# Performance work log

Hardware: AMD Instinct MI355X
Metric: run time of the kernel (lower is better)

## Reference

```python
import jax, jax.numpy as jnp
from jax import lax
import numpy as np

T, B, E, DENSE = 2048, 32, 512, 512
THRESH = 1.0
TAIL_MIN_W = 0.6
EPS = 1e-10


def setup_inputs() -> dict:
    key = jax.random.key(0)
    k1, k2, k3, k4 = jax.random.split(key, 4)
    encoder_raw_out = jax.random.normal(k1, (T, B, E), dtype=jnp.float32)  # T x B x C
    lengths = jax.random.randint(k2, (B,), T // 2, T + 1)
    padding_mask = jnp.arange(T)[None, :] >= lengths[:, None]  # [B,T], True = padding
    # xavier-uniform inits matching torch Linear helper
    s1 = float(np.sqrt(6.0 / (E + DENSE)))
    s2 = float(np.sqrt(6.0 / (DENSE + 1)))
    dense_w = jax.random.uniform(k3, (E, DENSE), jnp.float32, -s1, s1)
    dense_b = jnp.zeros((DENSE,), jnp.float32)
    wproj_w = jax.random.uniform(k4, (DENSE, 1), jnp.float32, -s2, s2)
    wproj_b = jnp.zeros((1,), jnp.float32)
    return dict(encoder_raw_out=encoder_raw_out, padding_mask=padding_mask,
                dense_w=dense_w, dense_b=dense_b, wproj_w=wproj_w, wproj_b=wproj_b)


def _cif(encoder_raw_out, padding_mask, dense_w, dense_b, wproj_w, wproj_b):
    x = jnp.transpose(encoder_raw_out, (1, 0, 2))  # [B,T,E]
    not_pad = ~padding_mask                         # [B,T]
    # produce_weight_type == 'dense'
    h = jax.nn.relu(jnp.einsum('bte,eu->btu', x, dense_w) + dense_b)
    weight = jax.nn.sigmoid(jnp.einsum('btu,uo->bto', h, wproj_w) + wproj_b)[..., 0]
    weight = weight * not_pad.astype(weight.dtype)  # [B,T]
    padding_start = not_pad.sum(-1)                 # [B] int

    def step(carry, inp):
        prev_w, prev_s = carry          # [B], [B,E]
        w_i, x_i, i = inp               # [B], [B,E], scalar
        fired = (prev_w + w_i) >= THRESH            # [B]
        remained = 1.0 - prev_w
        cur_w = jnp.where(fired, w_i - remained, w_i + prev_w)
        f = fired[:, None]
        cur_s = jnp.where(f, (w_i - remained)[:, None] * x_i,
                          prev_s + w_i[:, None] * x_i)
        fired_s = jnp.where(f, prev_s + remained[:, None] * x_i, 0.0)
        # tail handling (eval mode): at first padded frame, emit leftover if weighty enough
        at_tail = (i == padding_start)[:, None]
        tail_s = jnp.where(cur_w[:, None] <= TAIL_MIN_W, 0.0,
                           cur_s / (cur_w[:, None] + EPS))
        fired_s = jnp.where(at_tail, tail_s, fired_s)
        fired_s = jnp.where((i > padding_start)[:, None], 0.0, fired_s)
        return (cur_w, cur_s), fired_s

    init = (jnp.zeros((x.shape[0],), x.dtype), jnp.zeros_like(x[:, 0, :]))
    xs = (jnp.transpose(weight), encoder_raw_out, jnp.arange(x.shape[1]))
    _, fired_states = lax.scan(step, init, xs)          # [T,B,E]
    fired_states = jnp.transpose(fired_states, (1, 0, 2))  # [B,T,E]

    fired_marks = (jnp.abs(fired_states).sum(-1) != 0.0).astype(jnp.int32)  # [B,T]
    # left-pack fired states (non-fired rows are exact zeros, so they pad the tail)
    order = jnp.argsort(1 - fired_marks, axis=1, stable=True)               # [B,T]
    cif_out = jnp.take_along_axis(fired_states, order[:, :, None], axis=1)  # [B,T,E]
    cif_out_padding_mask = (jnp.abs(cif_out).sum(-1) != 0.0).astype(jnp.int32)
    quantity_out = weight.sum(-1)  # eval: org_weight == weight
    return cif_out, cif_out_padding_mask, quantity_out, fired_marks


def reference(encoder_raw_out, padding_mask, dense_w, dense_b, wproj_w, wproj_b):
    return _cif(encoder_raw_out, padding_mask, dense_w, dense_b, wproj_w, wproj_b)
```

## Files before the change

kernel.cpp:

```cpp
#include <hip/hip_runtime.h>
#include <math.h>

#define TT 2048
#define BB 32
#define EE 512
#define NN 512

typedef short bf16x8 __attribute__((ext_vector_type(8)));
typedef float f32x4 __attribute__((ext_vector_type(4)));

__device__ __forceinline__ short bf16_rne(float x) {
    const unsigned u = __float_as_uint(x);
    return (short)((u + 0x7FFFu + ((u >> 16) & 1u)) >> 16);
}
__device__ __forceinline__ float bf16_f32(short h) {
    return __uint_as_float(((unsigned)(unsigned short)h) << 16);
}
__device__ __forceinline__ void gload_lds16(const void* g, void* l) {
    __builtin_amdgcn_global_load_lds((const __attribute__((address_space(1))) void*)g,
                                     (__attribute__((address_space(3))) void*)l, 16, 0, 0);
}

__global__ void detect_mask_kernel(const unsigned* __restrict__ pm, int* __restrict__ flag) {
    __shared__ int s[1024];
    const int l = threadIdx.x;
    int bad = 0;
    for (int i = l; i < BB * TT; i += 1024) bad |= (pm[i] > 1u);
    s[l] = bad;
    __syncthreads();
    for (int st = 512; st > 0; st >>= 1) { if (l < st) s[l] |= s[l + st]; __syncthreads(); }
    if (l == 0) *flag = s[0];
}

__device__ __forceinline__ int pad_at(const void* pm, int idx, int isByte) {
    return isByte ? (int)(((const unsigned char*)pm)[idx] != 0)
                  : (int)(((const int*)pm)[idx] != 0);
}

__global__ void compute_ps_kernel(const void* __restrict__ pm, const int* __restrict__ flag,
                                  int* __restrict__ ps) {
    __shared__ int s[256];
    const int b = blockIdx.x, l = threadIdx.x;
    const int isByte = *flag;
    int cnt = 0;
    for (int t = l; t < TT; t += 256) cnt += (pad_at(pm, b * TT + t, isByte) == 0);
    s[l] = cnt;
    __syncthreads();
    for (int st = 128; st > 0; st >>= 1) { if (l < st) s[l] += s[l + st]; __syncthreads(); }
    if (l == 0) ps[b] = s[0];
}

__global__ __launch_bounds__(256) void split_w_kernel(const float* __restrict__ W,
                                                      short* __restrict__ Wh,
                                                      short* __restrict__ Wl) {
    __shared__ float tile[32][33];
    const int bn = blockIdx.x, bk = blockIdx.y;
    const int tx = threadIdx.x & 31, ty = threadIdx.x >> 5;
    for (int i = ty; i < 32; i += 8)
        tile[i][tx] = W[(size_t)(bk * 32 + i) * NN + bn * 32 + tx];
    __syncthreads();
    for (int i = ty; i < 32; i += 8) {
        const float val = tile[tx][i];
        const short h = bf16_rne(val);
        const short lo = bf16_rne(val - bf16_f32(h));
        const size_t o = (size_t)(bn * 32 + i) * EE + bk * 32 + tx;
        Wh[o] = h;
        Wl[o] = lo;
    }
}

__global__ __launch_bounds__(256, 2) void gemm_weight_mfma(
    const float* __restrict__ x, const void* __restrict__ pm, const int* __restrict__ flag,
    const short* __restrict__ Wh, const short* __restrict__ Wl,
    const float* __restrict__ bias, const float* __restrict__ v, const float* __restrict__ vb,
    float* __restrict__ weight_bt) {
    __shared__ __align__(16) short Ah[128 * 64];
    __shared__ __align__(16) short Al[128 * 64];
    __shared__ __align__(16) short Bh[128 * 64];
    __shared__ __align__(16) short Bl[128 * 64];
    __shared__ float bias_s[512], v_s[512];
    __shared__ float lsum[128][2];

    const int tid = threadIdx.x;
    const int l = tid & 63, wid = tid >> 6;
    const int wr = wid >> 1, wc = wid & 1;
    const int q = l >> 4, li = l & 15, x7 = l & 7;
    const int tp = blockIdx.x;

    for (int i = tid; i < 512; i += 256) { bias_s[i] = bias[i]; v_s[i] = v[i]; }

    const float* xblk = x + (size_t)tp * 128 * EE;
    const int arow = tid >> 1;
    const int akoff = (tid & 1) * 32;
    const int ac0 = akoff >> 3;
    const int aswz = arow & 7;

    float rowsum[4][4];
#pragma unroll
    for (int m = 0; m < 4; ++m)
#pragma unroll
        for (int r = 0; r < 4; ++r) rowsum[m][r] = 0.f;

    for (int nc = 0; nc < 4; ++nc) {
        const int n0 = nc * 128;
        f32x4 acc[4][4];
#pragma unroll
        for (int m = 0; m < 4; ++m)
#pragma unroll
            for (int n = 0; n < 4; ++n) acc[m][n] = (f32x4){0.f, 0.f, 0.f, 0.f};

        for (int k0 = 0; k0 < EE; k0 += 64) {
            __syncthreads();
#pragma unroll
            for (int i = 0; i < 4; ++i) {
                const int u = i * 256 + tid;
                const int row = u >> 3, c = u & 7;
                const int ge = (n0 + row) * EE + k0 + ((c ^ (row & 7)) << 3);
                gload_lds16(Wh + ge, &Bh[u * 8]);
                gload_lds16(Wl + ge, &Bl[u * 8]);
            }
            const float* xr = xblk + (size_t)arow * EE + k0 + akoff;
#pragma unroll
            for (int g = 0; g < 4; ++g) {
                float e[8];
                *(float4*)&e[0] = *(const float4*)&xr[g * 8];
                *(float4*)&e[4] = *(const float4*)&xr[g * 8 + 4];
                bf16x8 hv, lv;
#pragma unroll
                for (int j = 0; j < 8; ++j) {
                    const short h = bf16_rne(e[j]);
                    hv[j] = h;
                    lv[j] = bf16_rne(e[j] - bf16_f32(h));
                }
                const int p = arow * 64 + (((ac0 + g) ^ aswz) << 3);
                *(bf16x8*)&Ah[p] = hv;
                *(bf16x8*)&Al[p] = lv;
            }
            __syncthreads();
#pragma unroll
            for (int kf = 0; kf < 2; ++kf) {
                const int co = (((kf << 2) + q) ^ x7) << 3;
                bf16x8 ah[4], al[4];
#pragma unroll
                for (int m = 0; m < 4; ++m) {
                    const int ro = (wr * 64 + m * 16 + li) * 64 + co;
                    ah[m] = *(const bf16x8*)&Ah[ro];
                    al[m] = *(const bf16x8*)&Al[ro];
                }
#pragma unroll
                for (int n = 0; n < 4; ++n) {
                    const int bo = (wc * 64 + n * 16 + li) * 64 + co;
                    const bf16x8 bh = *(const bf16x8*)&Bh[bo];
                    const bf16x8 bl = *(const bf16x8*)&Bl[bo];
#pragma unroll
                    for (int m = 0; m < 4; ++m) {
                        acc[m][n] = __builtin_amdgcn_mfma_f32_16x16x32_bf16(ah[m], bh, acc[m][n], 0, 0, 0);
                        acc[m][n] = __builtin_amdgcn_mfma_f32_16x16x32_bf16(al[m], bh, acc[m][n], 0, 0, 0);
                        acc[m][n] = __builtin_amdgcn_mfma_f32_16x16x32_bf16(ah[m], bl, acc[m][n], 0, 0, 0);
                    }
                }
            }
        }
#pragma unroll
        for (int m = 0; m < 4; ++m)
#pragma unroll
            for (int n = 0; n < 4; ++n) {
                const int col = n0 + wc * 64 + n * 16 + li;
                const float bcol = bias_s[col], vcol = v_s[col];
#pragma unroll
                for (int r = 0; r < 4; ++r) {
                    const float h = fmaxf(acc[m][n][r] + bcol, 0.f);
                    rowsum[m][r] = fmaf(h, vcol, rowsum[m][r]);
                }
            }
    }
#pragma unroll
    for (int m = 0; m < 4; ++m)
#pragma unroll
        for (int r = 0; r < 4; ++r) {
            float s = rowsum[m][r];
            s += __shfl_xor(s, 1, 64);
            s += __shfl_xor(s, 2, 64);
            s += __shfl_xor(s, 4, 64);
            s += __shfl_xor(s, 8, 64);
            rowsum[m][r] = s;
        }
    if (li == 0) {
#pragma unroll
        for (int m = 0; m < 4; ++m)
#pragma unroll
            for (int r = 0; r < 4; ++r)
                lsum[wr * 64 + m * 16 + q * 4 + r][wc] = rowsum[m][r];
    }
    __syncthreads();
    if (tid < 128) {
        const int isByte = *flag;
        const float logit = lsum[tid][0] + lsum[tid][1] + *vb;
        const float wg = 1.0f / (1.0f + expf(-logit));
        const int gr = tp * 128 + tid;
        const int t = gr >> 5, b = gr & 31;
        weight_bt[(size_t)b * TT + t] = pad_at(pm, b * TT + t, isByte) ? 0.f : wg;
    }
}

#define BAND 5e-5f
#define MAXEV 32
__global__ __launch_bounds__(64) void cif_scan_kernel(
    float* __restrict__ weight_bt,
    const float* __restrict__ x, const float* __restrict__ W,
    const float* __restrict__ bias, const float* __restrict__ v,
    const float* __restrict__ vb,
    float* __restrict__ cseq_g) {
    __shared__ __align__(16) float wsm[TT];
    __shared__ __align__(16) float cseq[TT];
    __shared__ __align__(16) float xrow[EE];
    __shared__ int evl_s[MAXEV];
    __shared__ float wfix_s[MAXEV];
    __shared__ unsigned fixedbm[TT / 32];
    const int b = blockIdx.x, l = threadIdx.x;
    float* wrow = weight_bt + (size_t)b * TT;

    for (int t = l * 8; t < TT; t += 64 * 8) {
        *(float4*)&wsm[t]     = *(const float4*)&wrow[t];
        *(float4*)&wsm[t + 4] = *(const float4*)&wrow[t + 4];
    }
    fixedbm[l] = 0u;
    __syncthreads();

    int t0s = 0;
    for (int iter = 0; iter < 64; ++iter) {
        if (l == 0) {
            float c = (t0s > 0) ? cseq[t0s - 1] : 0.f;
            float4 n1a = *(const float4*)&wsm[t0s];
            float4 n1b = *(const float4*)&wsm[t0s + 4];
            const int tp8 = (t0s + 8) & (TT - 1);
            float4 n2a = *(const float4*)&wsm[tp8];
            float4 n2b = *(const float4*)&wsm[tp8 + 4];
            for (int t = t0s; t < TT; t += 8) {
                const float4 wa = n1a, wb = n1b;
                n1a = n2a; n1b = n2b;
                const int tn = (t + 16) & (TT - 1);
                n2a = *(const float4*)&wsm[tn];
                n2b = *(const float4*)&wsm[tn + 4];
                const float wv[8] = {wa.x, wa.y, wa.z, wa.w, wb.x, wb.y, wb.z, wb.w};
                float cs[8];
#pragma unroll
                for (int u = 0; u < 8; ++u) {
                    const float w = wv[u];
                    const float a = 1.0f - c;
                    const float s = c + w;
                    const float bb = w - a;
                    c = (s >= 1.0f) ? bb : s;
                    cs[u] = c;
                }
                *(float4*)&cseq[t]     = make_float4(cs[0], cs[1], cs[2], cs[3]);
                *(float4*)&cseq[t + 4] = make_float4(cs[4], cs[5], cs[6], cs[7]);
            }
        }
        __syncthreads();
        const int base = l * 32;
        const unsigned fixw = fixedbm[l];
        unsigned hm = 0u;
        for (int u = 0; u < 32; ++u) {
            const int t = base + u;
            const float w = wsm[t];
            if (w > 0.f && !((fixw >> u) & 1u)) {
                const float cprev = t ? cseq[t - 1] : 0.f;
                if (fabsf(cprev + w - 1.0f) < BAND) hm |= (1u << u);
            }
        }
        unsigned long long bal = __ballot(hm != 0u);
        int nev = 0;
        while (bal != 0ull && nev < MAXEV) {
            const int src = __ffsll((unsigned long long)bal) - 1;
            unsigned hs = __shfl(hm, src, 64);
            while (hs != 0u && nev < MAXEV) {
                const int u = __ffs(hs) - 1;
                if (l == 0) evl_s[nev] = src * 32 + u;
                ++nev;
                hs &= hs - 1u;
            }
            bal &= bal - 1ull;
        }
        __syncthreads();
        if (nev == 0) break;
        const float4 v0 = *(const float4*)&v[l * 8];
        const float4 v1 = *(const float4*)&v[l * 8 + 4];
        const float4 bi0 = *(const float4*)&bias[l * 8];
        const float4 bi1 = *(const float4*)&bias[l * 8 + 4];
        for (int k = 0; k < nev; ++k) {
            const int ev = evl_s[k];
            const float* xr = &x[((size_t)ev * BB + b) * EE];
            *(float4*)&xrow[l * 8]     = *(const float4*)&xr[l * 8];
            *(float4*)&xrow[l * 8 + 4] = *(const float4*)&xr[l * 8 + 4];
            __syncthreads();
            float h[8] = {bi0.x, bi0.y, bi0.z, bi0.w, bi1.x, bi1.y, bi1.z, bi1.w};
#pragma unroll 4
            for (int e = 0; e < EE; ++e) {
                const float xe = xrow[e];
                const float4 w0 = *(const float4*)&W[(size_t)e * NN + l * 8];
                const float4 w1 = *(const float4*)&W[(size_t)e * NN + l * 8 + 4];
                h[0] = fmaf(xe, w0.x, h[0]); h[1] = fmaf(xe, w0.y, h[1]);
                h[2] = fmaf(xe, w0.z, h[2]); h[3] = fmaf(xe, w0.w, h[3]);
                h[4] = fmaf(xe, w1.x, h[4]); h[5] = fmaf(xe, w1.y, h[5]);
                h[6] = fmaf(xe, w1.z, h[6]); h[7] = fmaf(xe, w1.w, h[7]);
            }
            float part = fmaxf(h[0], 0.f) * v0.x;
            part = fmaf(fmaxf(h[1], 0.f), v0.y, part);
            part = fmaf(fmaxf(h[2], 0.f), v0.z, part);
            part = fmaf(fmaxf(h[3], 0.f), v0.w, part);
            part = fmaf(fmaxf(h[4], 0.f), v1.x, part);
            part = fmaf(fmaxf(h[5], 0.f), v1.y, part);
            part = fmaf(fmaxf(h[6], 0.f), v1.z, part);
            part = fmaf(fmaxf(h[7], 0.f), v1.w, part);
#pragma unroll
            for (int s = 32; s >= 1; s >>= 1) part += __shfl_xor(part, s, 64);
            if (l == 0) wfix_s[k] = 1.0f / (1.0f + expf(-(part + *vb)));
            __syncthreads();
        }
        int firstflip = -1;
        for (int k = 0; k < nev; ++k) {
            const int ev = evl_s[k];
            const float wnew = wfix_s[k];
            const float cprev = ev ? cseq[ev - 1] : 0.f;
            const bool of = (cprev + wsm[ev]) >= 1.0f;
            const bool nf = (cprev + wnew) >= 1.0f;
            if (l == 0) {
                wsm[ev] = wnew;
                wrow[ev] = wnew;
                fixedbm[ev >> 5] |= (1u << (ev & 31));
            }
            if (nf != of && firstflip < 0) firstflip = ev;
        }
        __syncthreads();
        if (firstflip < 0) break;
        t0s = firstflip & ~7;
    }
    __syncthreads();
    for (int t = l * 8; t < TT; t += 64 * 8) {
        *(float4*)&cseq_g[(size_t)b * TT + t]     = *(const float4*)&cseq[t];
        *(float4*)&cseq_g[(size_t)b * TT + t + 4] = *(const float4*)&cseq[t + 4];
    }
}

__global__ __launch_bounds__(64) void cif_derive_kernel(
    const float* __restrict__ weight_bt, const float* __restrict__ cseq_g,
    const int* __restrict__ ps_arr,
    float* __restrict__ cc_bt, float4* __restrict__ recs,
    int* __restrict__ nfr, float* __restrict__ out_q, float* __restrict__ out_marks) {
    __shared__ __align__(16) float wsm[TT];
    __shared__ __align__(16) float cseq[TT];
    const int b = blockIdx.x, l = threadIdx.x;
    const int ps = ps_arr[b];
    for (int t = l * 8; t < TT; t += 64 * 8) {
        *(float4*)&wsm[t]      = *(const float4*)&weight_bt[(size_t)b * TT + t];
        *(float4*)&wsm[t + 4]  = *(const float4*)&weight_bt[(size_t)b * TT + t + 4];
        *(float4*)&cseq[t]     = *(const float4*)&cseq_g[(size_t)b * TT + t];
        *(float4*)&cseq[t + 4] = *(const float4*)&cseq_g[(size_t)b * TT + t + 4];
    }
    __syncthreads();

    const int base = l * 32;
    unsigned fmask = 0u;
    for (int u = 0; u < 32; ++u) {
        const int t = base + u;
        const float cprev = t ? cseq[t - 1] : 0.f;
        if (cprev + wsm[t] >= 1.0f) fmask |= (1u << u);
    }
    const int myF = __popc(fmask);
    int myLast = fmask ? (base + (31 - __clz(fmask))) : -1;

    int inc = myF;
#pragma unroll
    for (int off = 1; off < 64; off <<= 1) {
        const int n = __shfl_up(inc, off, 64);
        if (l >= off) inc += n;
    }
    const int exF = inc - myF;
    const int totF = __shfl(inc, 63, 64);
    int incLast = myLast;
#pragma unroll
    for (int off = 1; off < 64; off <<= 1) {
        const int n = __shfl_up(incLast, off, 64);
        if (l >= off) incLast = (incLast > n) ? incLast : n;
    }
    int prevFire = __shfl_up(incLast, 1, 64);
    if (l == 0) prevFire = -1;
    int tf = (prevFire > 0) ? prevFire : 0;

    int slot = exF;
    int tailWrote = 0;
    for (int u = 0; u < 32; ++u) {
        const int t = base + u;
        if (fmask & (1u << u)) {
            recs[(size_t)b * TT + slot] =
                make_float4(__int_as_float(tf), __int_as_float(t), cseq[tf], 1.0f);
            ++slot;
            tf = t;
        }
        if (t == ps) {
            const float cw = cseq[t];
            if (cw > 0.6f && totF < TT) {
                recs[(size_t)b * TT + totF] =
                    make_float4(__int_as_float(tf), __int_as_float(t - 1), cseq[tf],
                                1.0f / (cw + 1e-10f));
                tailWrote = 1;
            }
        }
    }
    const int tailAny = (__ballot(tailWrote) != 0ull) ? 1 : 0;

    float qpart = 0.f;
    for (int t = l; t < TT; t += 64) {
        const float w = wsm[t];
        const float cprev = t ? cseq[t - 1] : 0.f;
        const bool fired = (cprev + w) >= 1.0f;
        const float cc = fired ? (1.0f - cprev) : w;
        const bool tail = (t == ps) && (cseq[t] > 0.6f);
        cc_bt[(size_t)b * TT + t] = cc;
        out_marks[(size_t)b * TT + t] = (fired || tail) ? 1.f : 0.f;
        qpart += w;
    }
#pragma unroll
    for (int s = 32; s >= 1; s >>= 1) qpart += __shfl_xor(qpart, s, 64);
    if (l == 0) { out_q[b] = qpart; nfr[b] = totF + tailAny; }
}

__global__ __launch_bounds__(128) void cif_out_kernel(
    const float* __restrict__ x, const float* __restrict__ cc_bt,
    const float4* __restrict__ recs, const int* __restrict__ nfr,
    float* __restrict__ out_cif, float* __restrict__ out_mask) {
    const int j = blockIdx.x, b = blockIdx.y;
    const int l = threadIdx.x;
    const int m = nfr[b];
    float4 acc = make_float4(0.f, 0.f, 0.f, 0.f);
    const size_t obase = ((size_t)b * TT + j) * EE + l * 4;
    if (j < m) {
        const float4 r = recs[b * TT + j];
        const int t0 = __float_as_int(r.x);
        const int t1 = __float_as_int(r.y);
        const float fcoef = r.z, scale = r.w;
        for (int t = t0; t <= t1; ++t) {
            const float coeff = (t == t0) ? fcoef : cc_bt[(size_t)b * TT + t];
            const float4 xv = *(const float4*)&x[((size_t)t * BB + b) * EE + l * 4];
            acc.x = fmaf(coeff, xv.x, acc.x);
            acc.y = fmaf(coeff, xv.y, acc.y);
            acc.z = fmaf(coeff, xv.z, acc.z);
            acc.w = fmaf(coeff, xv.w, acc.w);
        }
        acc.x *= scale; acc.y *= scale; acc.z *= scale; acc.w *= scale;
        if (l == 0) out_mask[b * TT + j] = 1.f;
    } else {
        if (l == 0) out_mask[b * TT + j] = 0.f;
    }
    *(float4*)&out_cif[obase] = acc;
}

extern "C" void kernel_launch(void* const* d_in, const int* in_sizes, int n_in,
                              void* d_out, int out_size, void* d_ws, size_t ws_size,
                              hipStream_t stream) {
    const float* x    = (const float*)d_in[0];
    const void*  pm   = d_in[1];
    const float* W    = (const float*)d_in[2];
    const float* bias = (const float*)d_in[3];
    const float* v    = (const float*)d_in[4];
    const float* vb   = (const float*)d_in[5];

    float* ws        = (float*)d_ws;
    float* weight_bt = ws;
    float* cc_bt     = ws + (size_t)TT * BB;
    float4* recs     = (float4*)(ws + 2 * (size_t)TT * BB);
    int* nfr         = (int*)(ws + 2 * (size_t)TT * BB + 4 * (size_t)BB * TT);
    int* ps          = nfr + BB;
    int* flag        = ps + BB;

    float* out_cif   = (float*)d_out;
    float* out_mask  = out_cif + (size_t)BB * TT * EE;
    float* out_q     = out_mask + (size_t)BB * TT;
    float* out_marks = out_q + BB;

    short* Whs    = (short*)out_cif;
    short* Wls    = Whs + (size_t)NN * EE;
    float* cseq_g = (float*)((char*)out_cif + (2u << 20));

    detect_mask_kernel<<<1, 1024, 0, stream>>>((const unsigned*)pm, flag);
    compute_ps_kernel<<<BB, 256, 0, stream>>>(pm, flag, ps);
    split_w_kernel<<<dim3(16, 16), 256, 0, stream>>>(W, Whs, Wls);
    gemm_weight_mfma<<<512, 256, 0, stream>>>(x, pm, flag, Whs, Wls, bias, v, vb, weight_bt);
    cif_scan_kernel<<<BB, 64, 0, stream>>>(weight_bt, x, W, bias, v, vb, cseq_g);
    cif_derive_kernel<<<BB, 64, 0, stream>>>(weight_bt, cseq_g, ps, cc_bt, recs,
                                             nfr, out_q, out_marks);
    cif_out_kernel<<<dim3(TT, BB), 128, 0, stream>>>(x, cc_bt, recs, nfr, out_cif, out_mask);
}
```

Baseline: 490.0 us.

## Restructure weight GEMM: 512 threads, full-N per block, B fragments straight from global

The weight-producing GEMM now runs 8 waves per block, each owning a 64x128 slice across the full 512 output columns, so the activation tile is split into bf16 hi/lo only once instead of once per N chunk. W hi/lo fragments are read straight from global memory (L2-resident) instead of being staged through LDS, and the next activation k-slice is prefetched into registers. This removes the 4x repeated x conversion and the B LDS staging, but doubles accumulator registers per thread (32 f32x4) with launch bounds of 512 threads and 2 blocks, which risks spills or low occupancy. It also makes the MFMA loop depend on global-load latency for B.

```diff
diff --git a/kernel.cpp b/kernel.cpp
--- a/kernel.cpp
+++ b/kernel.cpp
@@ -15,10 +15,6 @@
 }
 __device__ __forceinline__ float bf16_f32(short h) {
     return __uint_as_float(((unsigned)(unsigned short)h) << 16);
-}
-__device__ __forceinline__ void gload_lds16(const void* g, void* l) {
-    __builtin_amdgcn_global_load_lds((const __attribute__((address_space(1))) void*)g,
-                                     (__attribute__((address_space(3))) void*)l, 16, 0, 0);
 }
 
 __global__ void detect_mask_kernel(const unsigned* __restrict__ pm, int* __restrict__ flag) {
@@ -69,111 +65,127 @@
     }
 }
 
-__global__ __launch_bounds__(256, 2) void gemm_weight_mfma(
+__global__ __launch_bounds__(512, 2) void gemm_weight_mfma(
     const float* __restrict__ x, const void* __restrict__ pm, const int* __restrict__ flag,
     const short* __restrict__ Wh, const short* __restrict__ Wl,
     const float* __restrict__ bias, const float* __restrict__ v, const float* __restrict__ vb,
     float* __restrict__ weight_bt) {
     __shared__ __align__(16) short Ah[128 * 64];
     __shared__ __align__(16) short Al[128 * 64];
-    __shared__ __align__(16) short Bh[128 * 64];
-    __shared__ __align__(16) short Bl[128 * 64];
     __shared__ float bias_s[512], v_s[512];
-    __shared__ float lsum[128][2];
+    __shared__ float lsum[128][4];
 
     const int tid = threadIdx.x;
     const int l = tid & 63, wid = tid >> 6;
-    const int wr = wid >> 1, wc = wid & 1;
+    const int wr = wid >> 2, wc = wid & 3;
     const int q = l >> 4, li = l & 15, x7 = l & 7;
     const int tp = blockIdx.x;
 
-    for (int i = tid; i < 512; i += 256) { bias_s[i] = bias[i]; v_s[i] = v[i]; }
+    bias_s[tid < 512 ? tid : 0] = bias[tid < 512 ? tid : 0];
+    v_s[tid < 512 ? tid : 0] = v[tid < 512 ? tid : 0];
 
     const float* xblk = x + (size_t)tp * 128 * EE;
-    const int arow = tid >> 1;
-    const int akoff = (tid & 1) * 32;
-    const int ac0 = akoff >> 3;
+    const int arow = tid >> 2;
+    const int kseg = (tid & 3) << 4;
+    const int c0 = (tid & 3) << 1;
     const int aswz = arow & 7;
 
-    float rowsum[4][4];
-#pragma unroll
-    for (int m = 0; m < 4; ++m)
-#pragma unroll
-        for (int r = 0; r < 4; ++r) rowsum[m][r] = 0.f;
-
-    for (int nc = 0; nc < 4; ++nc) {
-        const int n0 = nc * 128;
-        f32x4 acc[4][4];
+    f32x4 acc[2][4][4];
+#pragma unroll
+    for (int nc = 0; nc < 2; ++nc)
 #pragma unroll
         for (int m = 0; m < 4; ++m)
 #pragma unroll
-            for (int n = 0; n < 4; ++n) acc[m][n] = (f32x4){0.f, 0.f, 0.f, 0.f};
-
-        for (int k0 = 0; k0 < EE; k0 += 64) {
-            __syncthreads();
-#pragma unroll
-            for (int i = 0; i < 4; ++i) {
-                const int u = i * 256 + tid;
-                const int row = u >> 3, c = u & 7;
-                const int ge = (n0 + row) * EE + k0 + ((c ^ (row & 7)) << 3);
-                gload_lds16(Wh + ge, &Bh[u * 8]);
-                gload_lds16(Wl + ge, &Bl[u * 8]);
-            }
-            const float* xr = xblk + (size_t)arow * EE + k0 + akoff;
-#pragma unroll
-            for (int g = 0; g < 4; ++g) {
-                float e[8];
-                *(float4*)&e[0] = *(const float4*)&xr[g * 8];
-                *(float4*)&e[4] = *(const float4*)&xr[g * 8 + 4];
-                bf16x8 hv, lv;
-#pragma unroll
-                for (int j = 0; j < 8; ++j) {
-                    const short h = bf16_rne(e[j]);
-                    hv[j] = h;
-                    lv[j] = bf16_rne(e[j] - bf16_f32(h));
-                }
-                const int p = arow * 64 + (((ac0 + g) ^ aswz) << 3);
-                *(bf16x8*)&Ah[p] = hv;
-                *(bf16x8*)&Al[p] = lv;
-            }
-            __syncthreads();
-#pragma unroll
-            for (int kf = 0; kf < 2; ++kf) {
-                const int co = (((kf << 2) + q) ^ x7) << 3;
-                bf16x8 ah[4], al[4];
-#pragma unroll
-                for (int m = 0; m < 4; ++m) {
-                    const int ro = (wr * 64 + m * 16 + li) * 64 + co;
-                    ah[m] = *(const bf16x8*)&Ah[ro];
-                    al[m] = *(const bf16x8*)&Al[ro];
-                }
+            for (int n = 0; n < 4; ++n) acc[nc][m][n] = (f32x4){0.f, 0.f, 0.f, 0.f};
+
+    float4 p0, p1, p2, p3;
+    {
+        const float* xr = xblk + (size_t)arow * EE + kseg;
+        p0 = *(const float4*)&xr[0];
+        p1 = *(const float4*)&xr[4];
+        p2 = *(const float4*)&xr[8];
+        p3 = *(const float4*)&xr[12];
+    }
+
+    for (int ks = 0; ks < 8; ++ks) {
+        const int k0 = ks * 64;
+        float e[16];
+        *(float4*)&e[0]  = p0; *(float4*)&e[4]  = p1;
+        *(float4*)&e[8]  = p2; *(float4*)&e[12] = p3;
+        if (ks < 7) {
+            const float* xr = xblk + (size_t)arow * EE + (k0 + 64) + kseg;
+            p0 = *(const float4*)&xr[0];
+            p1 = *(const float4*)&xr[4];
+            p2 = *(const float4*)&xr[8];
+            p3 = *(const float4*)&xr[12];
+        }
+        bf16x8 hv0, lv0, hv1, lv1;
+#pragma unroll
+        for (int j = 0; j < 8; ++j) {
+            const short h = bf16_rne(e[j]);
+            hv0[j] = h;
+            lv0[j] = bf16_rne(e[j] - bf16_f32(h));
+        }
+#pragma unroll
+        for (int j = 0; j < 8; ++j) {
+            const short h = bf16_rne(e[8 + j]);
+            hv1[j] = h;
+            lv1[j] = bf16_rne(e[8 + j] - bf16_f32(h));
+        }
+        const int pa = arow * 64 + (((c0 + 0) ^ aswz) << 3);
+        const int pb = arow * 64 + (((c0 + 1) ^ aswz) << 3);
+        *(bf16x8*)&Ah[pa] = hv0; *(bf16x8*)&Al[pa] = lv0;
+        *(bf16x8*)&Ah[pb] = hv1; *(bf16x8*)&Al[pb] = lv1;
+        __syncthreads();
+#pragma unroll
+        for (int kf = 0; kf < 2; ++kf) {
+            const int co = (((kf << 2) + q) ^ x7) << 3;
+            bf16x8 ah[4], al[4];
+#pragma unroll
+            for (int m = 0; m < 4; ++m) {
+                const int ro = (wr * 64 + m * 16 + li) * 64 + co;
+                ah[m] = *(const bf16x8*)&Ah[ro];
+                al[m] = *(const bf16x8*)&Al[ro];
+            }
+            const int kk = k0 + (kf << 5) + (q << 3);
+#pragma unroll
+            for (int nc = 0; nc < 2; ++nc) {
 #pragma unroll
                 for (int n = 0; n < 4; ++n) {
-                    const int bo = (wc * 64 + n * 16 + li) * 64 + co;
-                    const bf16x8 bh = *(const bf16x8*)&Bh[bo];
-                    const bf16x8 bl = *(const bf16x8*)&Bl[bo];
+                    const int col = nc * 256 + wc * 64 + n * 16 + li;
+                    const size_t ga = (size_t)col * EE + kk;
+                    const bf16x8 bh = *(const bf16x8*)&Wh[ga];
+                    const bf16x8 bl = *(const bf16x8*)&Wl[ga];
 #pragma unroll
                     for (int m = 0; m < 4; ++m) {
-                        acc[m][n] = __builtin_amdgcn_mfma_f32_16x16x32_bf16(ah[m], bh, acc[m][n], 0, 0, 0);
-                        acc[m][n] = __builtin_amdgcn_mfma_f32_16x16x32_bf16(al[m], bh, acc[m][n], 0, 0, 0);
-                        acc[m][n] = __builtin_amdgcn_mfma_f32_16x16x32_bf16(ah[m], bl, acc[m][n], 0, 0, 0);
+                        acc[nc][m][n] = __builtin_amdgcn_mfma_f32_16x16x32_bf16(ah[m], bh, acc[nc][m][n], 0, 0, 0);
+                        acc[nc][m][n] = __builtin_amdgcn_mfma_f32_16x16x32_bf16(al[m], bh, acc[nc][m][n], 0, 0, 0);
+                        acc[nc][m][n] = __builtin_amdgcn_mfma_f32_16x16x32_bf16(ah[m], bl, acc[nc][m][n], 0, 0, 0);
                     }
                 }
             }
         }
+        __syncthreads();
+    }
+    float rowsum[4][4];
+#pragma unroll
+    for (int m = 0; m < 4; ++m)
+#pragma unroll
+        for (int r = 0; r < 4; ++r) rowsum[m][r] = 0.f;
+#pragma unroll
+    for (int nc = 0; nc < 2; ++nc)
 #pragma unroll
         for (int m = 0; m < 4; ++m)
 #pragma unroll
             for (int n = 0; n < 4; ++n) {
-                const int col = n0 + wc * 64 + n * 16 + li;
+                const int col = nc * 256 + wc * 64 + n * 16 + li;
                 const float bcol = bias_s[col], vcol = v_s[col];
 #pragma unroll
                 for (int r = 0; r < 4; ++r) {
-                    const float h = fmaxf(acc[m][n][r] + bcol, 0.f);
+                    const float h = fmaxf(acc[nc][m][n][r] + bcol, 0.f);
                     rowsum[m][r] = fmaf(h, vcol, rowsum[m][r]);
                 }
             }
-    }
 #pragma unroll
     for (int m = 0; m < 4; ++m)
 #pragma unroll
@@ -195,7 +207,8 @@
     __syncthreads();
     if (tid < 128) {
         const int isByte = *flag;
-        const float logit = lsum[tid][0] + lsum[tid][1] + *vb;
+        const float logit = ((lsum[tid][0] + lsum[tid][1]) +
+                             (lsum[tid][2] + lsum[tid][3])) + *vb;
         const float wg = 1.0f / (1.0f + expf(-logit));
         const int gr = tp * 128 + tid;
         const int t = gr >> 5, b = gr & 31;
@@ -486,7 +499,7 @@
     detect_mask_kernel<<<1, 1024, 0, stream>>>((const unsigned*)pm, flag);
     compute_ps_kernel<<<BB, 256, 0, stream>>>(pm, flag, ps);
     split_w_kernel<<<dim3(16, 16), 256, 0, stream>>>(W, Whs, Wls);
-    gemm_weight_mfma<<<512, 256, 0, stream>>>(x, pm, flag, Whs, Wls, bias, v, vb, weight_bt);
+    gemm_weight_mfma<<<512, 512, 0, stream>>>(x, pm, flag, Whs, Wls, bias, v, vb, weight_bt);
     cif_scan_kernel<<<BB, 64, 0, stream>>>(weight_bt, x, W, bias, v, vb, cseq_g);
     cif_derive_kernel<<<BB, 64, 0, stream>>>(weight_bt, cseq_g, ps, cc_bt, recs,
                                              nfr, out_q, out_marks);
```

Measured after the change: 606.7 us. 23.8% more time.
